# Kernel optimization log

Hardware: AMD Instinct MI355X
Metric: run time of the kernel (lower is better)

## Reference

```python
import jax, jax.numpy as jnp
import numpy as np

B, D, E, H, DEPTH, NH, K = 4, 384, 8, 1536, 12, 6, 2
P, NTOK = 16, 197  # patch size, 14*14 patches + cls
EPS = 1e-6


def layernorm(x, w, b):
    m = x.mean(-1, keepdims=True)
    v = ((x - m) ** 2).mean(-1, keepdims=True)
    return (x - m) / jnp.sqrt(v + EPS) * w + b


def attention(x, qkv_w, qkv_b, proj_w, proj_b):
    Bn, N, C = x.shape
    hd = C // NH
    qkv = x @ qkv_w.T + qkv_b                       # [B,N,3C]
    qkv = qkv.reshape(Bn, N, 3, NH, hd).transpose(2, 0, 3, 1, 4)
    q, k, v = qkv[0], qkv[1], qkv[2]                # [B,h,N,hd]
    attn = jax.nn.softmax((q @ k.transpose(0, 1, 3, 2)) * (hd ** -0.5), axis=-1)
    out = (attn @ v).transpose(0, 2, 1, 3).reshape(Bn, N, C)
    return out @ proj_w.T + proj_b


def mlp(x, w1, b1, w2, b2):
    h = jax.nn.gelu(x @ w1.T + b1, approximate=False)
    return h @ w2.T + b2


def moe_ffn(x2d, gw, w1, b1, w2, b2):
    # noiseless top-k gating (eval mode of NoisyTopKGating)
    logits = x2d @ gw                                # [T,E]
    T = logits.shape[0]
    top_vals, top_idx = jax.lax.top_k(logits, K + 1)
    gates_k = jax.nn.softmax(top_vals[:, :K], axis=-1)
    gates = jnp.zeros((T, E), x2d.dtype).at[jnp.arange(T)[:, None], top_idx[:, :K]].set(gates_k)
    # dense per-expert FFN, weighted combine (identical math to SparseDispatcher)
    h = jax.nn.gelu(jnp.einsum('td,edh->teh', x2d, w1) + b1, approximate=False)
    out = jnp.einsum('teh,ehd->ted', h, w2) + b2
    return jnp.einsum('te,ted->td', gates, out)


def forward(x, patch_w, patch_b, cls_token, pos_embed,
            ln1_w, ln1_b, qkv_w, qkv_b, proj_w, proj_b, ln2_w, ln2_b,
            fc1_w, fc1_b, fc2_w, fc2_b,
            gate_w, moe_w1, moe_b1, moe_w2, moe_b2, lnf_w, lnf_b):
    # patch embed: conv k=16 s=16
    feat = jax.lax.conv_general_dilated(x, patch_w, (P, P), 'VALID',
                                        dimension_numbers=('NCHW', 'OIHW', 'NCHW'))
    feat = feat + patch_b[None, :, None, None]
    Bn = feat.shape[0]
    tokens = feat.reshape(Bn, D, -1).transpose(0, 2, 1)          # [B,196,D]
    cls = jnp.broadcast_to(cls_token, (Bn, 1, D))
    h = jnp.concatenate([cls, tokens], axis=1) + pos_embed       # [B,197,D]

    for i in range(DEPTH):
        h = h + attention(layernorm(h, ln1_w[i], ln1_b[i]), qkv_w[i], qkv_b[i], proj_w[i], proj_b[i])
        y = layernorm(h, ln2_w[i], ln2_b[i])
        if i % 2 == 1:
            j = i // 2
            y2 = moe_ffn(y.reshape(-1, D), gate_w[j], moe_w1[j], moe_b1[j], moe_w2[j], moe_b2[j])
            h = h + y2.reshape(Bn, NTOK, D)
        else:
            j = i // 2
            h = h + mlp(y, fc1_w[j], fc1_b[j], fc2_w[j], fc2_b[j])
    return layernorm(h, lnf_w, lnf_b)


def setup_inputs() -> dict:
    key = jax.random.key(0)
    ks = jax.random.split(key, 16)
    rn = lambda k, s, sd=0.02: jax.random.normal(k, s, jnp.float32) * sd
    return {
        'x': jax.random.normal(ks[0], (B, 3, 224, 224), jnp.float32),
        'patch_w': rn(ks[1], (D, 3, P, P)), 'patch_b': jnp.zeros((D,), jnp.float32),
        'cls_token': rn(ks[2], (1, 1, D)), 'pos_embed': rn(ks[3], (1, NTOK, D)),
        'ln1_w': jnp.ones((DEPTH, D), jnp.float32), 'ln1_b': jnp.zeros((DEPTH, D), jnp.float32),
        'qkv_w': rn(ks[4], (DEPTH, 3 * D, D)), 'qkv_b': jnp.zeros((DEPTH, 3 * D), jnp.float32),
        'proj_w': rn(ks[5], (DEPTH, D, D)), 'proj_b': jnp.zeros((DEPTH, D), jnp.float32),
        'ln2_w': jnp.ones((DEPTH, D), jnp.float32), 'ln2_b': jnp.zeros((DEPTH, D), jnp.float32),
        'fc1_w': rn(ks[6], (DEPTH // 2, H, D)), 'fc1_b': jnp.zeros((DEPTH // 2, H), jnp.float32),
        'fc2_w': rn(ks[7], (DEPTH // 2, D, H)), 'fc2_b': jnp.zeros((DEPTH // 2, D), jnp.float32),
        'gate_w': rn(ks[8], (DEPTH // 2, D, E)),
        'moe_w1': rn(ks[9], (DEPTH // 2, E, D, H)), 'moe_b1': jnp.zeros((DEPTH // 2, E, H), jnp.float32),
        'moe_w2': rn(ks[10], (DEPTH // 2, E, H, D)), 'moe_b2': jnp.zeros((DEPTH // 2, E, D), jnp.float32),
        'lnf_w': jnp.ones((D,), jnp.float32), 'lnf_b': jnp.zeros((D,), jnp.float32),
    }


def reference(x, patch_w, patch_b, cls_token, pos_embed,
              ln1_w, ln1_b, qkv_w, qkv_b, proj_w, proj_b, ln2_w, ln2_b,
              fc1_w, fc1_b, fc2_w, fc2_b,
              gate_w, moe_w1, moe_b1, moe_w2, moe_b2, lnf_w, lnf_b):
    return forward(x, patch_w, patch_b, cls_token, pos_embed,
                   ln1_w, ln1_b, qkv_w, qkv_b, proj_w, proj_b, ln2_w, ln2_b,
                   fc1_w, fc1_b, fc2_w, fc2_b,
                   gate_w, moe_w1, moe_b1, moe_w2, moe_b2, lnf_w, lnf_b)
```

## Files before the change

kernel.cpp:

```cpp
#include <hip/hip_runtime.h>
#include <math.h>

#define NBATCH 4
#define NTOK 197
#define TT 788
#define DM 384
#define HM 1536
#define NHEAD 6
#define NEXP 8
#define LD2 72
#define MOUTSZ (TT * 2 * DM)

typedef __attribute__((ext_vector_type(8))) short bf16x8;
typedef __attribute__((ext_vector_type(4))) float f32x4;

__device__ __forceinline__ void f2bf2(float x, short& hi, short& lo) {
    unsigned u = __float_as_uint(x);
    unsigned uh = u + (0x7fffu + ((u >> 16) & 1u));
    hi = (short)(uh >> 16);
    float hf = __uint_as_float(uh & 0xffff0000u);
    float r = x - hf;
    unsigned v = __float_as_uint(r);
    lo = (short)((v + (0x7fffu + ((v >> 16) & 1u))) >> 16);
}
__device__ __forceinline__ float gelu_f(float x) {
    return 0.5f * x * (1.0f + erff(x * 0.7071067811865475f));
}

__global__ void k_im2col(const float* __restrict__ X, float* __restrict__ P) {
    int p = blockIdx.x;
    int b = p / 196, pp = p % 196;
    int py = pp / 14, px = pp % 14;
    const float* xb = X + (size_t)b * 3 * 224 * 224;
    float* dst = P + (size_t)p * 768;
    for (int idx = threadIdx.x; idx < 768; idx += 256) {
        int c = idx >> 8;
        int i = (idx >> 4) & 15;
        int j = idx & 15;
        dst[idx] = xb[((size_t)c * 224 + py * 16 + i) * 224 + px * 16 + j];
    }
}

__global__ void k_assemble(const float* __restrict__ PO, const float* __restrict__ pb,
                           const float* __restrict__ cls, const float* __restrict__ pos,
                           float* __restrict__ H) {
    int t = blockIdx.x;
    int b = t / NTOK, n = t % NTOK;
    for (int d = threadIdx.x; d < DM; d += 128) {
        float v;
        if (n == 0) v = cls[d];
        else v = PO[((size_t)b * 196 + (n - 1)) * DM + d] + pb[d];
        H[(size_t)t * DM + d] = v + pos[(size_t)n * DM + d];
    }
}

__global__ void k_ln(const float* __restrict__ X, const float* __restrict__ w,
                     const float* __restrict__ b, float* __restrict__ Y) {
    int t = blockIdx.x, lane = threadIdx.x;
    const float* x = X + (size_t)t * DM;
    float v[6];
    float s = 0.f;
    #pragma unroll
    for (int i = 0; i < 6; ++i) { v[i] = x[lane + i * 64]; s += v[i]; }
    #pragma unroll
    for (int off = 32; off; off >>= 1) s += __shfl_xor(s, off);
    float mean = s * (1.f / 384.f);
    float q = 0.f;
    #pragma unroll
    for (int i = 0; i < 6; ++i) { float d = v[i] - mean; q += d * d; }
    #pragma unroll
    for (int off = 32; off; off >>= 1) q += __shfl_xor(q, off);
    float inv = rsqrtf(q * (1.f / 384.f) + 1e-6f);
    float* y = Y + (size_t)t * DM;
    #pragma unroll
    for (int i = 0; i < 6; ++i) {
        int d = lane + i * 64;
        y[d] = (v[i] - mean) * inv * w[d] + b[d];
    }
}

__global__ __launch_bounds__(256) void k_gemm_mfma(
    const float* __restrict__ A, const float* __restrict__ W,
    const float* __restrict__ bias, float* __restrict__ C,
    int M, int N, int K, int flags, int MT, int NT, int wprot,
    const float* __restrict__ lnw, const float* __restrict__ lnb)
{
    int mt, nt;
    {
        int lane8 = blockIdx.x & 7;
        int idx = blockIdx.x >> 3;
        if (wprot) {
            mt = idx % MT;
            nt = lane8 + 8 * (idx / MT);
            if (nt >= NT) return;
        } else {
            nt = idx % NT;
            mt = lane8 + 8 * (idx / NT);
            if (mt >= MT) return;
        }
    }
    __shared__ short Ah[64 * LD2], Al[64 * LD2], Bh[64 * LD2], Bl[64 * LD2];
    const int bm = mt * 64, bn = nt * 64;
    const int tid = threadIdx.x;
    const int lane = tid & 63, w = tid >> 6;
    const int wr = w >> 1, wc = w & 1;
    const int r16 = lane & 15, g = lane >> 4;
    const int sr = tid >> 4;
    const int sc = (tid & 15) * 4;
    const bool doln = (flags & 8) != 0;
    float am[4], ai[4];
    #pragma unroll
    for (int p = 0; p < 4; ++p) { am[p] = 0.f; ai[p] = 1.f; }
    if (doln) {
        int j = tid & 15;
        #pragma unroll
        for (int p = 0; p < 4; ++p) {
            int r = bm + sr + p * 16;
            if (r < M) {
                const float* xr = A + (size_t)r * K;
                float s = 0.f, ss = 0.f;
                #pragma unroll
                for (int i = 0; i < 6; ++i) {
                    float4 v = *(const float4*)(xr + j * 4 + i * 64);
                    s += v.x + v.y + v.z + v.w;
                    ss += v.x * v.x + v.y * v.y + v.z * v.z + v.w * v.w;
                }
                #pragma unroll
                for (int off = 1; off < 16; off <<= 1) {
                    s += __shfl_xor(s, off);
                    ss += __shfl_xor(ss, off);
                }
                float mean = s * (1.f / 384.f);
                float var = ss * (1.f / 384.f) - mean * mean;
                am[p] = mean;
                ai[p] = rsqrtf(var + 1e-6f);
            }
        }
    }
    float4 ra[4], rb[4], lw4, lb4;
    auto LOADT = [&](int k0) {
        if (doln) {
            lw4 = *(const float4*)(lnw + k0 + sc);
            lb4 = *(const float4*)(lnb + k0 + sc);
        }
        #pragma unroll
        for (int p = 0; p < 4; ++p) {
            int r = sr + p * 16;
            ra[p] = make_float4(0.f, 0.f, 0.f, 0.f);
            if (bm + r < M) ra[p] = *(const float4*)(A + (size_t)(bm + r) * K + k0 + sc);
            rb[p] = *(const float4*)(W + (size_t)(bn + r) * K + k0 + sc);
        }
    };
    auto STORET = [&]() {
        #pragma unroll
        for (int p = 0; p < 4; ++p) {
            int r = sr + p * 16;
            float4 a4 = ra[p];
            if (doln) {
                a4.x = (a4.x - am[p]) * ai[p] * lw4.x + lb4.x;
                a4.y = (a4.y - am[p]) * ai[p] * lw4.y + lb4.y;
                a4.z = (a4.z - am[p]) * ai[p] * lw4.z + lb4.z;
                a4.w = (a4.w - am[p]) * ai[p] * lw4.w + lb4.w;
            }
            float4 b4 = rb[p];
            short4 ah, al, bh, bl;
            f2bf2(a4.x, ah.x, al.x); f2bf2(a4.y, ah.y, al.y);
            f2bf2(a4.z, ah.z, al.z); f2bf2(a4.w, ah.w, al.w);
            f2bf2(b4.x, bh.x, bl.x); f2bf2(b4.y, bh.y, bl.y);
            f2bf2(b4.z, bh.z, bl.z); f2bf2(b4.w, bh.w, bl.w);
            *(short4*)&Ah[r * LD2 + sc] = ah; *(short4*)&Al[r * LD2 + sc] = al;
            *(short4*)&Bh[r * LD2 + sc] = bh; *(short4*)&Bl[r * LD2 + sc] = bl;
        }
    };
    f32x4 acc[2][2] = {};
    auto COMPUTE = [&]() {
        #pragma unroll
        for (int kk = 0; kk < 2; ++kk) {
            bf16x8 afh[2], afl[2], bfh[2], bfl[2];
            #pragma unroll
            for (int i = 0; i < 2; ++i) {
                int off = (wr * 32 + i * 16 + r16) * LD2 + kk * 32 + g * 8;
                afh[i] = *(const bf16x8*)&Ah[off];
                afl[i] = *(const bf16x8*)&Al[off];
            }
            #pragma unroll
            for (int j = 0; j < 2; ++j) {
                int off = (wc * 32 + j * 16 + r16) * LD2 + kk * 32 + g * 8;
                bfh[j] = *(const bf16x8*)&Bh[off];
                bfl[j] = *(const bf16x8*)&Bl[off];
            }
            #pragma unroll
            for (int i = 0; i < 2; ++i)
                #pragma unroll
                for (int j = 0; j < 2; ++j) {
                    acc[i][j] = __builtin_amdgcn_mfma_f32_16x16x32_bf16(afl[i], bfh[j], acc[i][j], 0, 0, 0);
                    acc[i][j] = __builtin_amdgcn_mfma_f32_16x16x32_bf16(afh[i], bfl[j], acc[i][j], 0, 0, 0);
                    acc[i][j] = __builtin_amdgcn_mfma_f32_16x16x32_bf16(afh[i], bfh[j], acc[i][j], 0, 0, 0);
                }
        }
    };
    LOADT(0);
    STORET();
    __syncthreads();
    for (int k0 = 64; k0 < K; k0 += 64) {
        LOADT(k0);
        COMPUTE();
        __syncthreads();
        STORET();
        __syncthreads();
    }
    COMPUTE();
    #pragma unroll
    for (int i = 0; i < 2; ++i) {
        #pragma unroll
        for (int j = 0; j < 2; ++j) {
            int n = bn + wc * 32 + j * 16 + r16;
            float bb = bias ? bias[n] : 0.f;
            int mbase = bm + wr * 32 + i * 16 + g * 4;
            #pragma unroll
            for (int r = 0; r < 4; ++r) {
                int m = mbase + r;
                if (m < M) {
                    float v = acc[i][j][r] + bb;
                    if (flags & 1) v = gelu_f(v);
                    float* cp = C + (size_t)m * N + n;
                    if (flags & 2) v += *cp;
                    *cp = v;
                }
            }
        }
    }
}

__global__ __launch_bounds__(256) void k_scoresm(const float* __restrict__ QKV,
                                                 float* __restrict__ S) {
    int z = blockIdx.y;
    int b = z / NHEAD, hh = z % NHEAD;
    int i0 = blockIdx.x * 32;
    __shared__ float qs[32][65];
    __shared__ float ks[32][65];
    __shared__ float srow[32][200];
    int tid = threadIdx.x;
    int r = tid >> 3, d0 = (tid & 7) * 8, c0 = (tid & 7) * 4, l8 = tid & 7;
    {
        float4 v0 = make_float4(0,0,0,0), v1 = v0;
        if (i0 + r < NTOK) {
            const float* qp = QKV + ((size_t)(b * NTOK + i0 + r)) * 1152 + hh * 64 + d0;
            v0 = *(const float4*)qp; v1 = *(const float4*)(qp + 4);
        }
        qs[r][d0+0]=v0.x; qs[r][d0+1]=v0.y; qs[r][d0+2]=v0.z; qs[r][d0+3]=v0.w;
        qs[r][d0+4]=v1.x; qs[r][d0+5]=v1.y; qs[r][d0+6]=v1.z; qs[r][d0+7]=v1.w;
    }
    if (l8 == 0) { srow[r][197] = -1e30f; srow[r][198] = -1e30f; srow[r][199] = -1e30f; }
    for (int j0 = 0; j0 < NTOK; j0 += 32) {
        __syncthreads();
        {
            float4 v0 = make_float4(0,0,0,0), v1 = v0;
            if (j0 + r < NTOK) {
                const float* kp = QKV + ((size_t)(b * NTOK + j0 + r)) * 1152 + 384 + hh * 64 + d0;
                v0 = *(const float4*)kp; v1 = *(const float4*)(kp + 4);
            }
            ks[r][d0+0]=v0.x; ks[r][d0+1]=v0.y; ks[r][d0+2]=v0.z; ks[r][d0+3]=v0.w;
            ks[r][d0+4]=v1.x; ks[r][d0+5]=v1.y; ks[r][d0+6]=v1.z; ks[r][d0+7]=v1.w;
        }
        __syncthreads();
        float acc[4] = {0.f, 0.f, 0.f, 0.f};
        #pragma unroll 8
        for (int d = 0; d < 64; ++d) {
            float qv = qs[r][d];
            #pragma unroll
            for (int u = 0; u < 4; ++u) acc[u] += qv * ks[c0 + u][d];
        }
        #pragma unroll
        for (int u = 0; u < 4; ++u) {
            int j = j0 + c0 + u;
            if (j < NTOK) srow[r][j] = acc[u] * 0.125f;
        }
    }
    __syncthreads();
    float m = -1e30f;
    for (int c = l8; c < 200; c += 8) m = fmaxf(m, srow[r][c]);
    #pragma unroll
    for (int off = 1; off < 8; off <<= 1) m = fmaxf(m, __shfl_xor(m, off));
    float s = 0.f;
    for (int c = l8; c < 200; c += 8) {
        float e = expf(srow[r][c] - m);
        srow[r][c] = e;
        s += e;
    }
    #pragma unroll
    for (int off = 1; off < 8; off <<= 1) s += __shfl_xor(s, off);
    float invs = 1.f / s;
    int i = i0 + r;
    if (i < NTOK) {
        float* sp = S + ((size_t)z * NTOK + i) * NTOK;
        for (int c = l8; c < NTOK; c += 8) sp[c] = srow[r][c] * invs;
    }
}

__global__ __launch_bounds__(256) void k_pv(const float* __restrict__ S, const float* __restrict__ QKV,
                                            float* __restrict__ AO) {
    int z = blockIdx.y;
    int b = z / NHEAD, hh = z % NHEAD;
    int i0 = blockIdx.x * 32;
    __shared__ float ps[32][33];
    __shared__ float vs[32][65];
    int tid = threadIdx.x;
    int r = tid >> 3;
    int c4 = (tid & 7) * 4;
    int d0 = (tid & 7) * 8;
    float acc[8] = {};
    for (int k0 = 0; k0 < NTOK; k0 += 32) {
        #pragma unroll
        for (int u = 0; u < 4; ++u) {
            int i = i0 + r, j = k0 + c4 + u;
            ps[r][c4 + u] = (i < NTOK && j < NTOK) ? S[((size_t)z * NTOK + i) * NTOK + j] : 0.f;
        }
        {
            float4 v0 = make_float4(0,0,0,0), v1 = v0;
            if (k0 + r < NTOK) {
                const float* vp = QKV + ((size_t)(b * NTOK + k0 + r)) * 1152 + 768 + hh * 64 + d0;
                v0 = *(const float4*)vp; v1 = *(const float4*)(vp + 4);
            }
            vs[r][d0+0]=v0.x; vs[r][d0+1]=v0.y; vs[r][d0+2]=v0.z; vs[r][d0+3]=v0.w;
            vs[r][d0+4]=v1.x; vs[r][d0+5]=v1.y; vs[r][d0+6]=v1.z; vs[r][d0+7]=v1.w;
        }
        __syncthreads();
        #pragma unroll 8
        for (int kk = 0; kk < 32; ++kk) {
            float pw = ps[r][kk];
            #pragma unroll
            for (int j = 0; j < 8; ++j) acc[j] += pw * vs[kk][d0 + j];
        }
        __syncthreads();
    }
    int i = i0 + r;
    if (i < NTOK) {
        float* op = AO + (size_t)(b * NTOK + i) * DM + hh * 64 + d0;
        #pragma unroll
        for (int j = 0; j < 8; ++j) op[j] = acc[j];
    }
}

__global__ void k_route_ln(const float* __restrict__ H, float* __restrict__ lnstat,
                           const float* __restrict__ lnw, const float* __restrict__ lnb,
                           const float* __restrict__ GW,
                           int* __restrict__ eidx, float* __restrict__ egate) {
    int t = blockIdx.x * 4 + (threadIdx.x >> 6);
    if (t >= TT) return;
    int lane = threadIdx.x & 63;
    const float* x = H + (size_t)t * DM;
    float v[6];
    float s = 0.f, ss = 0.f;
    #pragma unroll
    for (int i = 0; i < 6; ++i) {
        v[i] = x[lane + i * 64];
        s += v[i];
        ss += v[i] * v[i];
    }
    #pragma unroll
    for (int off = 32; off; off >>= 1) { s += __shfl_xor(s, off); ss += __shfl_xor(ss, off); }
    float mean = s * (1.f / 384.f);
    float var = ss * (1.f / 384.f) - mean * mean;
    float inv = rsqrtf(var + 1e-6f);
    if (lane == 0) { lnstat[2 * t] = mean; lnstat[2 * t + 1] = inv; }
    float l8[NEXP] = {};
    #pragma unroll
    for (int i = 0; i < 6; ++i) {
        int d = lane + i * 64;
        float yv = (v[i] - mean) * inv * lnw[d] + lnb[d];
        const float* g = GW + (size_t)d * NEXP;
        #pragma unroll
        for (int e = 0; e < NEXP; ++e) l8[e] += yv * g[e];
    }
    #pragma unroll
    for (int e = 0; e < NEXP; ++e) {
        float vv = l8[e];
        #pragma unroll
        for (int off = 32; off; off >>= 1) vv += __shfl_xor(vv, off);
        l8[e] = vv;
    }
    if (lane == 0) {
        int b0 = 0;
        #pragma unroll
        for (int e = 1; e < NEXP; ++e) if (l8[e] > l8[b0]) b0 = e;
        int b1 = -1;
        #pragma unroll
        for (int e = 0; e < NEXP; ++e) if (e != b0 && (b1 < 0 || l8[e] > l8[b1])) b1 = e;
        float e1 = expf(l8[b1] - l8[b0]);
        float denom = 1.f + e1;
        eidx[2 * t] = b0; eidx[2 * t + 1] = b1;
        egate[2 * t] = 1.f / denom; egate[2 * t + 1] = e1 / denom;
    }
}

__global__ void k_pscatter(int* __restrict__ cnt, int* __restrict__ basep,
                           const int* __restrict__ eidx,
                           int* __restrict__ slot_tok, int* __restrict__ slot_of) {
    __shared__ int hist[NEXP];
    __shared__ int bp[NEXP];
    __shared__ int fl[NEXP];
    int tid = threadIdx.x;
    if (tid < NEXP) { hist[tid] = 0; fl[tid] = 0; }
    __syncthreads();
    for (int i = tid; i < 2 * TT; i += 256) atomicAdd(&hist[eidx[i]], 1);
    __syncthreads();
    if (tid == 0) {
        int s = 0;
        for (int e = 0; e < NEXP; ++e) { bp[e] = s; s += hist[e]; }
    }
    __syncthreads();
    if (tid < NEXP) { cnt[tid] = hist[tid]; basep[tid] = bp[tid]; }
    for (int t = tid; t < TT; t += 256) {
        #pragma unroll
        for (int k = 0; k < 2; ++k) {
            int e = eidx[2 * t + k];
            int pos = atomicAdd(&fl[e], 1);
            int s = bp[e] + pos;
            slot_tok[s] = t;
            slot_of[2 * t + k] = s;
        }
    }
}

__global__ __launch_bounds__(256) void k_moe1_mfma(
    const float* __restrict__ H, const float* __restrict__ lnstat,
    const float* __restrict__ lnw, const float* __restrict__ lnb,
    const float* __restrict__ W1, const float* __restrict__ B1,
    const int* __restrict__ slot_tok, const int* __restrict__ cnt, const int* __restrict__ basep,
    float* __restrict__ HID)
{
    const int e = blockIdx.x & 7;
    const int idx = blockIdx.x >> 3;
    const int mt = idx % 25;
    const int nt = idx / 25;
    const int c = cnt[e];
    const int r0 = mt * 64;
    if (r0 >= c) return;
    const int sbase = basep[e];
    const int n0 = nt * 64;
    const float* W = W1 + (size_t)e * DM * HM;
    const float* B1e = B1 + (size_t)e * HM;
    __shared__ short Ah[64 * LD2], Al[64 * LD2], Bh[64 * LD2], Bl[64 * LD2];
    const int tid = threadIdx.x;
    const int lane = tid & 63, w = tid >> 6;
    const int wr = w >> 1, wc = w & 1;
    const int r16 = lane & 15, g = lane >> 4;
    const int sr = tid >> 4, sc = (tid & 15) * 4;
    const int kq = (tid >> 4) * 4;
    int tokp[4];
    float am4[4], ai4[4];
    #pragma unroll
    for (int p = 0; p < 4; ++p) {
        int m = r0 + sr + p * 16;
        tokp[p] = (m < c) ? slot_tok[sbase + m] : -1;
        am4[p] = 0.f; ai4[p] = 1.f;
        if (tokp[p] >= 0) { am4[p] = lnstat[2 * tokp[p]]; ai4[p] = lnstat[2 * tokp[p] + 1]; }
    }
    f32x4 acc[2][2] = {};
    for (int k0 = 0; k0 < DM; k0 += 64) {
        float4 lw4 = *(const float4*)(lnw + k0 + sc);
        float4 lb4 = *(const float4*)(lnb + k0 + sc);
        #pragma unroll
        for (int p = 0; p < 4; ++p) {
            int r = sr + p * 16;
            float4 a4 = make_float4(0.f, 0.f, 0.f, 0.f);
            if (tokp[p] >= 0) {
                a4 = *(const float4*)(H + (size_t)tokp[p] * DM + k0 + sc);
                a4.x = (a4.x - am4[p]) * ai4[p] * lw4.x + lb4.x;
                a4.y = (a4.y - am4[p]) * ai4[p] * lw4.y + lb4.y;
                a4.z = (a4.z - am4[p]) * ai4[p] * lw4.z + lb4.z;
                a4.w = (a4.w - am4[p]) * ai4[p] * lw4.w + lb4.w;
            }
            short4 ah, al;
            f2bf2(a4.x, ah.x, al.x); f2bf2(a4.y, ah.y, al.y);
            f2bf2(a4.z, ah.z, al.z); f2bf2(a4.w, ah.w, al.w);
            *(short4*)&Ah[r * LD2 + sc] = ah; *(short4*)&Al[r * LD2 + sc] = al;
        }
        {
            float4 b4[4];
            #pragma unroll
            for (int i = 0; i < 4; ++i)
                b4[i] = *(const float4*)(W + (size_t)(k0 + kq + i) * HM + n0 + sc);
            float col[4][4] = {
                { b4[0].x, b4[1].x, b4[2].x, b4[3].x },
                { b4[0].y, b4[1].y, b4[2].y, b4[3].y },
                { b4[0].z, b4[1].z, b4[2].z, b4[3].z },
                { b4[0].w, b4[1].w, b4[2].w, b4[3].w } };
            #pragma unroll
            for (int u = 0; u < 4; ++u) {
                short4 hh, ll;
                f2bf2(col[u][0], hh.x, ll.x); f2bf2(col[u][1], hh.y, ll.y);
                f2bf2(col[u][2], hh.z, ll.z); f2bf2(col[u][3], hh.w, ll.w);
                *(short4*)&Bh[(sc + u) * LD2 + kq] = hh;
                *(short4*)&Bl[(sc + u) * LD2 + kq] = ll;
            }
        }
        __syncthreads();
        #pragma unroll
        for (int kk = 0; kk < 2; ++kk) {
            bf16x8 afh[2], afl[2], bfh[2], bfl[2];
            #pragma unroll
            for (int i = 0; i < 2; ++i) {
                int off = (wr * 32 + i * 16 + r16) * LD2 + kk * 32 + g * 8;
                afh[i] = *(const bf16x8*)&Ah[off];
                afl[i] = *(const bf16x8*)&Al[off];
            }
            #pragma unroll
            for (int j = 0; j < 2; ++j) {
                int off = (wc * 32 + j * 16 + r16) * LD2 + kk * 32 + g * 8;
                bfh[j] = *(const bf16x8*)&Bh[off];
                bfl[j] = *(const bf16x8*)&Bl[off];
            }
            #pragma unroll
            for (int i = 0; i < 2; ++i)
                #pragma unroll
                for (int j = 0; j < 2; ++j) {
                    acc[i][j] = __builtin_amdgcn_mfma_f32_16x16x32_bf16(afl[i], bfh[j], acc[i][j], 0, 0, 0);
                    acc[i][j] = __builtin_amdgcn_mfma_f32_16x16x32_bf16(afh[i], bfl[j], acc[i][j], 0, 0, 0);
                    acc[i][j] = __builtin_amdgcn_mfma_f32_16x16x32_bf16(afh[i], bfh[j], acc[i][j], 0, 0, 0);
                }
        }
        __syncthreads();
    }
    #pragma unroll
    for (int i = 0; i < 2; ++i) {
        #pragma unroll
        for (int j = 0; j < 2; ++j) {
            int n = n0 + wc * 32 + j * 16 + r16;
            float bb = B1e[n];
            #pragma unroll
            for (int r = 0; r < 4; ++r) {
                int m = r0 + wr * 32 + i * 16 + g * 4 + r;
                if (m < c)
                    HID[(size_t)(sbase + m) * HM + n] = gelu_f(acc[i][j][r] + bb);
            }
        }
    }
}

__global__ __launch_bounds__(256) void k_moe2_mfma(
    const float* __restrict__ HID, const float* __restrict__ W2,
    const int* __restrict__ cnt, const int* __restrict__ basep,
    float* __restrict__ MOUTP)
{
    const int e = blockIdx.x & 7;
    const int idx = blockIdx.x >> 3;
    const int mt = idx % 25;
    const int rest = idx / 25;
    const int nt = rest % 6;
    const int ks = rest / 6;
    const int c = cnt[e];
    const int r0 = mt * 64;
    if (r0 >= c) return;
    const int sbase = basep[e];
    const int n0 = nt * 64;
    const int kbase = ks * 384;
    const float* W = W2 + (size_t)e * HM * DM + (size_t)kbase * DM;
    float* outp = MOUTP + (size_t)ks * MOUTSZ;
    __shared__ short Ah[64 * LD2], Al[64 * LD2], Bh[64 * LD2], Bl[64 * LD2];
    const int tid = threadIdx.x;
    const int lane = tid & 63, w = tid >> 6;
    const int wr = w >> 1, wc = w & 1;
    const int r16 = lane & 15, g = lane >> 4;
    const int sr = tid >> 4, sc = (tid & 15) * 4;
    const int kq = (tid >> 4) * 4;
    f32x4 acc[2][2] = {};
    for (int k0 = 0; k0 < 384; k0 += 64) {
        #pragma unroll
        for (int p = 0; p < 4; ++p) {
            int r = sr + p * 16;
            int m = r0 + r;
            float4 a4 = make_float4(0.f, 0.f, 0.f, 0.f);
            if (m < c) a4 = *(const float4*)(HID + (size_t)(sbase + m) * HM + kbase + k0 + sc);
            short4 ah, al;
            f2bf2(a4.x, ah.x, al.x); f2bf2(a4.y, ah.y, al.y);
            f2bf2(a4.z, ah.z, al.z); f2bf2(a4.w, ah.w, al.w);
            *(short4*)&Ah[r * LD2 + sc] = ah; *(short4*)&Al[r * LD2 + sc] = al;
        }
        {
            float4 b4[4];
            #pragma unroll
            for (int i = 0; i < 4; ++i)
                b4[i] = *(const float4*)(W + (size_t)(k0 + kq + i) * DM + n0 + sc);
            float col[4][4] = {
                { b4[0].x, b4[1].x, b4[2].x, b4[3].x },
                { b4[0].y, b4[1].y, b4[2].y, b4[3].y },
                { b4[0].z, b4[1].z, b4[2].z, b4[3].z },
                { b4[0].w, b4[1].w, b4[2].w, b4[3].w } };
            #pragma unroll
            for (int u = 0; u < 4; ++u) {
                short4 hh, ll;
                f2bf2(col[u][0], hh.x, ll.x); f2bf2(col[u][1], hh.y, ll.y);
                f2bf2(col[u][2], hh.z, ll.z); f2bf2(col[u][3], hh.w, ll.w);
                *(short4*)&Bh[(sc + u) * LD2 + kq] = hh;
                *(short4*)&Bl[(sc + u) * LD2 + kq] = ll;
            }
        }
        __syncthreads();
        #pragma unroll
        for (int kk = 0; kk < 2; ++kk) {
            bf16x8 afh[2], afl[2], bfh[2], bfl[2];
            #pragma unroll
            for (int i = 0; i < 2; ++i) {
                int off = (wr * 32 + i * 16 + r16) * LD2 + kk * 32 + g * 8;
                afh[i] = *(const bf16x8*)&Ah[off];
                afl[i] = *(const bf16x8*)&Al[off];
            }
            #pragma unroll
            for (int j = 0; j < 2; ++j) {
                int off = (wc * 32 + j * 16 + r16) * LD2 + kk * 32 + g * 8;
                bfh[j] = *(const bf16x8*)&Bh[off];
                bfl[j] = *(const bf16x8*)&Bl[off];
            }
            #pragma unroll
            for (int i = 0; i < 2; ++i)
                #pragma unroll
                for (int j = 0; j < 2; ++j) {
                    acc[i][j] = __builtin_amdgcn_mfma_f32_16x16x32_bf16(afl[i], bfh[j], acc[i][j], 0, 0, 0);
                    acc[i][j] = __builtin_amdgcn_mfma_f32_16x16x32_bf16(afh[i], bfl[j], acc[i][j], 0, 0, 0);
                    acc[i][j] = __builtin_amdgcn_mfma_f32_16x16x32_bf16(afh[i], bfh[j], acc[i][j], 0, 0, 0);
                }
        }
        __syncthreads();
    }
    #pragma unroll
    for (int i = 0; i < 2; ++i) {
        #pragma unroll
        for (int j = 0; j < 2; ++j) {
            int n = n0 + wc * 32 + j * 16 + r16;
            #pragma unroll
            for (int r = 0; r < 4; ++r) {
                int m = r0 + wr * 32 + i * 16 + g * 4 + r;
                if (m < c)
                    outp[(size_t)(sbase + m) * DM + n] = acc[i][j][r];
            }
        }
    }
}

__global__ void k_combine(const float* __restrict__ MOUTP, const int* __restrict__ slot_of,
                          const int* __restrict__ eidx, const float* __restrict__ egate,
                          const float* __restrict__ B2, float* __restrict__ H) {
    int t = blockIdx.x;
    int s0 = slot_of[2 * t], s1 = slot_of[2 * t + 1];
    int e0 = eidx[2 * t], e1 = eidx[2 * t + 1];
    float g0 = egate[2 * t], g1 = egate[2 * t + 1];
    for (int d = threadIdx.x; d < DM; d += 128) {
        float v0 = B2[(size_t)e0 * DM + d];
        float v1 = B2[(size_t)e1 * DM + d];
        #pragma unroll
        for (int p = 0; p < 4; ++p) {
            v0 += MOUTP[(size_t)p * MOUTSZ + (size_t)s0 * DM + d];
            v1 += MOUTP[(size_t)p * MOUTSZ + (size_t)s1 * DM + d];
        }
        H[(size_t)t * DM + d] += g0 * v0 + g1 * v1;
    }
}

extern "C" void kernel_launch(void* const* d_in, const int* in_sizes, int n_in,
                              void* d_out, int out_size, void* d_ws, size_t ws_size,
                              hipStream_t stream) {
    const float* x         = (const float*)d_in[0];
    const float* patch_w   = (const float*)d_in[1];
    const float* patch_b   = (const float*)d_in[2];
    const float* cls_token = (const float*)d_in[3];
    const float* pos_embed = (const float*)d_in[4];
    const float* ln1_w     = (const float*)d_in[5];
    const float* ln1_b     = (const float*)d_in[6];
    const float* qkv_w     = (const float*)d_in[7];
    const float* qkv_b     = (const float*)d_in[8];
    const float* proj_w    = (const float*)d_in[9];
    const float* proj_b    = (const float*)d_in[10];
    const float* ln2_w     = (const float*)d_in[11];
    const float* ln2_b     = (const float*)d_in[12];
    const float* fc1_w     = (const float*)d_in[13];
    const float* fc1_b     = (const float*)d_in[14];
    const float* fc2_w     = (const float*)d_in[15];
    const float* fc2_b     = (const float*)d_in[16];
    const float* gate_w    = (const float*)d_in[17];
    const float* moe_w1    = (const float*)d_in[18];
    const float* moe_b1    = (const float*)d_in[19];
    const float* moe_w2    = (const float*)d_in[20];
    const float* moe_b2    = (const float*)d_in[21];
    const float* lnf_w     = (const float*)d_in[22];
    const float* lnf_b     = (const float*)d_in[23];
    float* out = (float*)d_out;

    float* wsf = (float*)d_ws;
    float* regA     = wsf;
    float* patches  = regA;
    float* patchout = regA + 602112;
    float* moehid   = regA;
    float* h     = regA + 2420736;
    float* spare = h + 302592;
    float* qkvb  = spare + 302592;
    float* attno = qkvb + 907776;
    float* regC  = attno + 302592;
    float* S    = regC;
    float* hid  = regC;
    float* mout4 = qkvb;
    float* egate = regC + 1210368;
    int* ib       = (int*)(egate + 1576);
    int* eidx     = ib;
    int* slot_tok = ib + 1576;
    int* slot_of  = ib + 3152;
    int* cnt      = ib + 4728;
    int* basep    = ib + 4736;
    float* lnstat = (float*)(ib + 4752);

    k_im2col<<<784, 256, 0, stream>>>(x, patches);
    k_gemm_mfma<<<96, 256, 0, stream>>>(patches, patch_w, nullptr, patchout,
                                        784, DM, 768, 0, 13, 6, 0, nullptr, nullptr);
    k_assemble<<<TT, 128, 0, stream>>>(patchout, patch_b, cls_token, pos_embed, h);

    for (int l = 0; l < 12; ++l) {
        k_gemm_mfma<<<312, 256, 0, stream>>>(h, qkv_w + (size_t)l * 1152 * DM,
                                             qkv_b + l * 1152, qkvb, TT, 1152, DM, 8,
                                             13, 18, 1,
                                             ln1_w + l * DM, ln1_b + l * DM);
        k_scoresm<<<dim3(7, NBATCH * NHEAD), 256, 0, stream>>>(qkvb, S);
        k_pv<<<dim3(7, NBATCH * NHEAD), 256, 0, stream>>>(S, qkvb, attno);
        k_gemm_mfma<<<96, 256, 0, stream>>>(attno, proj_w + (size_t)l * DM * DM,
                                            proj_b + l * DM, h, TT, DM, DM, 2,
                                            13, 6, 0, nullptr, nullptr);
        int j = l >> 1;
        if ((l & 1) == 0) {
            k_gemm_mfma<<<312, 256, 0, stream>>>(h, fc1_w + (size_t)j * HM * DM,
                                                 fc1_b + j * HM, hid, TT, HM, DM, 9,
                                                 13, 24, 1,
                                                 ln2_w + l * DM, ln2_b + l * DM);
            k_gemm_mfma<<<96, 256, 0, stream>>>(hid, fc2_w + (size_t)j * DM * HM,
                                                fc2_b + j * DM, h, TT, DM, HM, 2,
                                                13, 6, 0, nullptr, nullptr);
        } else {
            k_route_ln<<<197, 256, 0, stream>>>(h, lnstat, ln2_w + l * DM, ln2_b + l * DM,
                                                gate_w + (size_t)j * DM * NEXP, eidx, egate);
            k_pscatter<<<1, 256, 0, stream>>>(cnt, basep, eidx, slot_tok, slot_of);
            k_moe1_mfma<<<8 * 25 * 24, 256, 0, stream>>>(
                h, lnstat, ln2_w + l * DM, ln2_b + l * DM,
                moe_w1 + (size_t)j * NEXP * DM * HM, moe_b1 + (size_t)j * NEXP * HM,
                slot_tok, cnt, basep, moehid);
            k_moe2_mfma<<<8 * 25 * 24, 256, 0, stream>>>(
                moehid, moe_w2 + (size_t)j * NEXP * HM * DM, cnt, basep, mout4);
            k_combine<<<TT, 128, 0, stream>>>(mout4, slot_of, eidx, egate,
                                              moe_b2 + (size_t)j * NEXP * DM, h);
        }
    }
    k_ln<<<TT, 64, 0, stream>>>(h, lnf_w, lnf_b, out);
}
```

Measured before the change: 1.787 ms.

## Fuse attention scores, softmax and PV into one online-softmax kernel

Replaces the separate scores+softmax kernel and PV kernel with a single flash-style kernel. It keeps a running max and sum per query row, rescales the PV accumulator for each 32-key tile, and reuses one shared buffer for K and then V. This removes the write and re-read of the full probability matrix in global memory and one launch per layer, at the cost of extra exp and rescale work per tile. Separately, the MoE expert GEMM grids shrink from 25 to 13 row tiles per expert, since no expert can receive more than 788 tokens, which cuts the number of blocks that launch only to exit.

```diff
diff --git a/kernel.cpp b/kernel.cpp
--- a/kernel.cpp
+++ b/kernel.cpp
@@ -232,16 +232,19 @@
     }
 }
 
-__global__ __launch_bounds__(256) void k_scoresm(const float* __restrict__ QKV,
-                                                 float* __restrict__ S) {
+__global__ __launch_bounds__(256) void k_fattn(const float* __restrict__ QKV,
+                                               float* __restrict__ AO) {
     int z = blockIdx.y;
     int b = z / NHEAD, hh = z % NHEAD;
     int i0 = blockIdx.x * 32;
     __shared__ float qs[32][65];
-    __shared__ float ks[32][65];
-    __shared__ float srow[32][200];
+    __shared__ float kv[32][65];
+    __shared__ float sc[32][33];
     int tid = threadIdx.x;
-    int r = tid >> 3, d0 = (tid & 7) * 8, c0 = (tid & 7) * 4, l8 = tid & 7;
+    int r = tid >> 3;
+    int l8 = tid & 7;
+    int d0 = l8 * 8;
+    int c0 = l8 * 4;
     {
         float4 v0 = make_float4(0,0,0,0), v1 = v0;
         if (i0 + r < NTOK) {
@@ -251,7 +254,8 @@
         qs[r][d0+0]=v0.x; qs[r][d0+1]=v0.y; qs[r][d0+2]=v0.z; qs[r][d0+3]=v0.w;
         qs[r][d0+4]=v1.x; qs[r][d0+5]=v1.y; qs[r][d0+6]=v1.z; qs[r][d0+7]=v1.w;
     }
-    if (l8 == 0) { srow[r][197] = -1e30f; srow[r][198] = -1e30f; srow[r][199] = -1e30f; }
+    float accv[8] = {};
+    float mrow = -1e30f, lrow = 0.f;
     for (int j0 = 0; j0 < NTOK; j0 += 32) {
         __syncthreads();
         {
@@ -260,85 +264,65 @@
                 const float* kp = QKV + ((size_t)(b * NTOK + j0 + r)) * 1152 + 384 + hh * 64 + d0;
                 v0 = *(const float4*)kp; v1 = *(const float4*)(kp + 4);
             }
-            ks[r][d0+0]=v0.x; ks[r][d0+1]=v0.y; ks[r][d0+2]=v0.z; ks[r][d0+3]=v0.w;
-            ks[r][d0+4]=v1.x; ks[r][d0+5]=v1.y; ks[r][d0+6]=v1.z; ks[r][d0+7]=v1.w;
-        }
-        __syncthreads();
-        float acc[4] = {0.f, 0.f, 0.f, 0.f};
+            kv[r][d0+0]=v0.x; kv[r][d0+1]=v0.y; kv[r][d0+2]=v0.z; kv[r][d0+3]=v0.w;
+            kv[r][d0+4]=v1.x; kv[r][d0+5]=v1.y; kv[r][d0+6]=v1.z; kv[r][d0+7]=v1.w;
+        }
+        __syncthreads();
+        float a0 = 0.f, a1 = 0.f, a2 = 0.f, a3 = 0.f;
         #pragma unroll 8
         for (int d = 0; d < 64; ++d) {
             float qv = qs[r][d];
-            #pragma unroll
-            for (int u = 0; u < 4; ++u) acc[u] += qv * ks[c0 + u][d];
-        }
+            a0 += qv * kv[c0 + 0][d];
+            a1 += qv * kv[c0 + 1][d];
+            a2 += qv * kv[c0 + 2][d];
+            a3 += qv * kv[c0 + 3][d];
+        }
+        float s4[4];
+        s4[0] = (j0 + c0 + 0 < NTOK) ? a0 * 0.125f : -1e30f;
+        s4[1] = (j0 + c0 + 1 < NTOK) ? a1 * 0.125f : -1e30f;
+        s4[2] = (j0 + c0 + 2 < NTOK) ? a2 * 0.125f : -1e30f;
+        s4[3] = (j0 + c0 + 3 < NTOK) ? a3 * 0.125f : -1e30f;
+        float tmax = fmaxf(fmaxf(s4[0], s4[1]), fmaxf(s4[2], s4[3]));
+        #pragma unroll
+        for (int off = 1; off < 8; off <<= 1) tmax = fmaxf(tmax, __shfl_xor(tmax, off));
+        float mnew = fmaxf(mrow, tmax);
+        float scale = expf(mrow - mnew);
+        float tsum = 0.f;
         #pragma unroll
         for (int u = 0; u < 4; ++u) {
-            int j = j0 + c0 + u;
-            if (j < NTOK) srow[r][j] = acc[u] * 0.125f;
-        }
-    }
-    __syncthreads();
-    float m = -1e30f;
-    for (int c = l8; c < 200; c += 8) m = fmaxf(m, srow[r][c]);
-    #pragma unroll
-    for (int off = 1; off < 8; off <<= 1) m = fmaxf(m, __shfl_xor(m, off));
-    float s = 0.f;
-    for (int c = l8; c < 200; c += 8) {
-        float e = expf(srow[r][c] - m);
-        srow[r][c] = e;
-        s += e;
-    }
-    #pragma unroll
-    for (int off = 1; off < 8; off <<= 1) s += __shfl_xor(s, off);
-    float invs = 1.f / s;
-    int i = i0 + r;
-    if (i < NTOK) {
-        float* sp = S + ((size_t)z * NTOK + i) * NTOK;
-        for (int c = l8; c < NTOK; c += 8) sp[c] = srow[r][c] * invs;
-    }
-}
-
-__global__ __launch_bounds__(256) void k_pv(const float* __restrict__ S, const float* __restrict__ QKV,
-                                            float* __restrict__ AO) {
-    int z = blockIdx.y;
-    int b = z / NHEAD, hh = z % NHEAD;
-    int i0 = blockIdx.x * 32;
-    __shared__ float ps[32][33];
-    __shared__ float vs[32][65];
-    int tid = threadIdx.x;
-    int r = tid >> 3;
-    int c4 = (tid & 7) * 4;
-    int d0 = (tid & 7) * 8;
-    float acc[8] = {};
-    for (int k0 = 0; k0 < NTOK; k0 += 32) {
-        #pragma unroll
-        for (int u = 0; u < 4; ++u) {
-            int i = i0 + r, j = k0 + c4 + u;
-            ps[r][c4 + u] = (i < NTOK && j < NTOK) ? S[((size_t)z * NTOK + i) * NTOK + j] : 0.f;
-        }
+            float e = expf(s4[u] - mnew);
+            sc[r][c0 + u] = e;
+            tsum += e;
+        }
+        #pragma unroll
+        for (int off = 1; off < 8; off <<= 1) tsum += __shfl_xor(tsum, off);
+        lrow = lrow * scale + tsum;
+        mrow = mnew;
+        #pragma unroll
+        for (int j = 0; j < 8; ++j) accv[j] *= scale;
+        __syncthreads();
         {
             float4 v0 = make_float4(0,0,0,0), v1 = v0;
-            if (k0 + r < NTOK) {
-                const float* vp = QKV + ((size_t)(b * NTOK + k0 + r)) * 1152 + 768 + hh * 64 + d0;
+            if (j0 + r < NTOK) {
+                const float* vp = QKV + ((size_t)(b * NTOK + j0 + r)) * 1152 + 768 + hh * 64 + d0;
                 v0 = *(const float4*)vp; v1 = *(const float4*)(vp + 4);
             }
-            vs[r][d0+0]=v0.x; vs[r][d0+1]=v0.y; vs[r][d0+2]=v0.z; vs[r][d0+3]=v0.w;
-            vs[r][d0+4]=v1.x; vs[r][d0+5]=v1.y; vs[r][d0+6]=v1.z; vs[r][d0+7]=v1.w;
+            kv[r][d0+0]=v0.x; kv[r][d0+1]=v0.y; kv[r][d0+2]=v0.z; kv[r][d0+3]=v0.w;
+            kv[r][d0+4]=v1.x; kv[r][d0+5]=v1.y; kv[r][d0+6]=v1.z; kv[r][d0+7]=v1.w;
         }
         __syncthreads();
         #pragma unroll 8
         for (int kk = 0; kk < 32; ++kk) {
-            float pw = ps[r][kk];
-            #pragma unroll
-            for (int j = 0; j < 8; ++j) acc[j] += pw * vs[kk][d0 + j];
-        }
-        __syncthreads();
-    }
-    int i = i0 + r;
-    if (i < NTOK) {
-        float* op = AO + (size_t)(b * NTOK + i) * DM + hh * 64 + d0;
-        #pragma unroll
-        for (int j = 0; j < 8; ++j) op[j] = acc[j];
+            float pw = sc[r][kk];
+            #pragma unroll
+            for (int j = 0; j < 8; ++j) accv[j] += pw * kv[kk][d0 + j];
+        }
+    }
+    if (i0 + r < NTOK) {
+        float inv = 1.f / lrow;
+        float* op = AO + (size_t)(b * NTOK + i0 + r) * DM + hh * 64 + d0;
+        #pragma unroll
+        for (int j = 0; j < 8; ++j) op[j] = accv[j] * inv;
     }
 }
 
@@ -432,8 +416,8 @@
 {
     const int e = blockIdx.x & 7;
     const int idx = blockIdx.x >> 3;
-    const int mt = idx % 25;
-    const int nt = idx / 25;
+    const int mt = idx % 13;
+    const int nt = idx / 13;
     const int c = cnt[e];
     const int r0 = mt * 64;
     if (r0 >= c) return;
@@ -546,8 +530,8 @@
 {
     const int e = blockIdx.x & 7;
     const int idx = blockIdx.x >> 3;
-    const int mt = idx % 25;
-    const int rest = idx / 25;
+    const int mt = idx % 13;
+    const int rest = idx / 13;
     const int nt = rest % 6;
     const int ks = rest / 6;
     const int c = cnt[e];
@@ -697,7 +681,6 @@
     float* qkvb  = spare + 302592;
     float* attno = qkvb + 907776;
     float* regC  = attno + 302592;
-    float* S    = regC;
     float* hid  = regC;
     float* mout4 = qkvb;
     float* egate = regC + 1210368;
@@ -719,8 +702,7 @@
                                              qkv_b + l * 1152, qkvb, TT, 1152, DM, 8,
                                              13, 18, 1,
                                              ln1_w + l * DM, ln1_b + l * DM);
-        k_scoresm<<<dim3(7, NBATCH * NHEAD), 256, 0, stream>>>(qkvb, S);
-        k_pv<<<dim3(7, NBATCH * NHEAD), 256, 0, stream>>>(S, qkvb, attno);
+        k_fattn<<<dim3(7, NBATCH * NHEAD), 256, 0, stream>>>(qkvb, attno);
         k_gemm_mfma<<<96, 256, 0, stream>>>(attno, proj_w + (size_t)l * DM * DM,
                                             proj_b + l * DM, h, TT, DM, DM, 2,
                                             13, 6, 0, nullptr, nullptr);
@@ -737,11 +719,11 @@
             k_route_ln<<<197, 256, 0, stream>>>(h, lnstat, ln2_w + l * DM, ln2_b + l * DM,
                                                 gate_w + (size_t)j * DM * NEXP, eidx, egate);
             k_pscatter<<<1, 256, 0, stream>>>(cnt, basep, eidx, slot_tok, slot_of);
-            k_moe1_mfma<<<8 * 25 * 24, 256, 0, stream>>>(
+            k_moe1_mfma<<<8 * 13 * 24, 256, 0, stream>>>(
                 h, lnstat, ln2_w + l * DM, ln2_b + l * DM,
                 moe_w1 + (size_t)j * NEXP * DM * HM, moe_b1 + (size_t)j * NEXP * HM,
                 slot_tok, cnt, basep, moehid);
-            k_moe2_mfma<<<8 * 25 * 24, 256, 0, stream>>>(
+            k_moe2_mfma<<<8 * 13 * 24, 256, 0, stream>>>(
                 moehid, moe_w2 + (size_t)j * NEXP * HM * DM, cnt, basep, mout4);
             k_combine<<<TT, 128, 0, stream>>>(mout4, slot_of, eidx, egate,
                                               moe_b2 + (size_t)j * NEXP * DM, h);
```

New measurement: 1.807 ms. About the same (+1.1%).

## Replace LDS-tiled GEMM with single-wave register GEMM and trim MoE grids

Applied to the files above, without the earlier changes.

The dense GEMM used for patch embedding, QKV, proj and the MLP layers is replaced by a one-wavefront kernel on 32x32 tiles. Each lane loads its MFMA operand fragments straight from global memory into double-buffered registers, so there is no LDS staging and no block barriers. This launches several times more blocks, which addresses the poor CU occupancy of the earlier 96- and 312-block grids. The cost is that operand reuse now depends on L2 instead of shared memory, so more global loads are issued. Separately, the MoE expert kernels now launch 13 row tiles per expert instead of 25, enough to cover the 788-token maximum, which removes blocks that only exited early.

```diff
diff --git a/kernel.cpp b/kernel.cpp
--- a/kernel.cpp
+++ b/kernel.cpp
@@ -79,7 +79,9 @@
     }
 }
 
-__global__ __launch_bounds__(256) void k_gemm_mfma(
+struct FR { float4 a00, a01, a10, a11, b00, b01, b10, b11; };
+
+__global__ __launch_bounds__(64) void k_gemm_rw(
     const float* __restrict__ A, const float* __restrict__ W,
     const float* __restrict__ bias, float* __restrict__ C,
     int M, int N, int K, int flags, int MT, int NT, int wprot,
@@ -99,124 +101,108 @@
             if (mt >= MT) return;
         }
     }
-    __shared__ short Ah[64 * LD2], Al[64 * LD2], Bh[64 * LD2], Bl[64 * LD2];
-    const int bm = mt * 64, bn = nt * 64;
-    const int tid = threadIdx.x;
-    const int lane = tid & 63, w = tid >> 6;
-    const int wr = w >> 1, wc = w & 1;
+    const int bm = mt * 32, bn = nt * 32;
+    const int lane = threadIdx.x;
     const int r16 = lane & 15, g = lane >> 4;
-    const int sr = tid >> 4;
-    const int sc = (tid & 15) * 4;
+    const int rA0 = bm + r16, rA1 = bm + 16 + r16;
+    const bool a0ok = rA0 < M, a1ok = rA1 < M;
+    const float* ap0 = A + (size_t)rA0 * K;
+    const float* ap1 = A + (size_t)rA1 * K;
+    const float* bp0 = W + (size_t)(bn + r16) * K;
+    const float* bp1 = W + (size_t)(bn + 16 + r16) * K;
     const bool doln = (flags & 8) != 0;
-    float am[4], ai[4];
-    #pragma unroll
-    for (int p = 0; p < 4; ++p) { am[p] = 0.f; ai[p] = 1.f; }
+    float am0 = 0.f, ai0 = 1.f, am1 = 0.f, ai1 = 1.f;
     if (doln) {
-        int j = tid & 15;
-        #pragma unroll
-        for (int p = 0; p < 4; ++p) {
-            int r = bm + sr + p * 16;
-            if (r < M) {
-                const float* xr = A + (size_t)r * K;
-                float s = 0.f, ss = 0.f;
-                #pragma unroll
-                for (int i = 0; i < 6; ++i) {
-                    float4 v = *(const float4*)(xr + j * 4 + i * 64);
-                    s += v.x + v.y + v.z + v.w;
-                    ss += v.x * v.x + v.y * v.y + v.z * v.z + v.w * v.w;
-                }
-                #pragma unroll
-                for (int off = 1; off < 16; off <<= 1) {
-                    s += __shfl_xor(s, off);
-                    ss += __shfl_xor(ss, off);
-                }
-                float mean = s * (1.f / 384.f);
-                float var = ss * (1.f / 384.f) - mean * mean;
-                am[p] = mean;
-                ai[p] = rsqrtf(var + 1e-6f);
-            }
-        }
-    }
-    float4 ra[4], rb[4], lw4, lb4;
-    auto LOADT = [&](int k0) {
+        int row = bm + (lane & 31);
+        float s = 0.f, ss = 0.f;
+        if (row < M) {
+            const float* xr = A + (size_t)row * 384 + (lane >> 5) * 192;
+            #pragma unroll
+            for (int i = 0; i < 48; ++i) {
+                float4 v = *(const float4*)(xr + i * 4);
+                s += v.x + v.y + v.z + v.w;
+                ss += v.x * v.x + v.y * v.y + v.z * v.z + v.w * v.w;
+            }
+        }
+        s += __shfl_xor(s, 32);
+        ss += __shfl_xor(ss, 32);
+        float mean = s * (1.f / 384.f);
+        float var = ss * (1.f / 384.f) - mean * mean;
+        float inv = rsqrtf(var + 1e-6f);
+        am0 = __shfl(mean, r16);      ai0 = __shfl(inv, r16);
+        am1 = __shfl(mean, r16 + 16); ai1 = __shfl(inv, r16 + 16);
+    }
+    f32x4 acc[2][2] = {};
+
+    auto LOAD = [&](int k0, FR& R) {
+        int kc = k0 + g * 8;
+        float4 z = make_float4(0.f, 0.f, 0.f, 0.f);
+        R.a00 = a0ok ? *(const float4*)(ap0 + kc) : z;
+        R.a01 = a0ok ? *(const float4*)(ap0 + kc + 4) : z;
+        R.a10 = a1ok ? *(const float4*)(ap1 + kc) : z;
+        R.a11 = a1ok ? *(const float4*)(ap1 + kc + 4) : z;
+        R.b00 = *(const float4*)(bp0 + kc);
+        R.b01 = *(const float4*)(bp0 + kc + 4);
+        R.b10 = *(const float4*)(bp1 + kc);
+        R.b11 = *(const float4*)(bp1 + kc + 4);
+    };
+    auto COMP = [&](int k0, const FR& R) {
+        float av0[8] = { R.a00.x, R.a00.y, R.a00.z, R.a00.w, R.a01.x, R.a01.y, R.a01.z, R.a01.w };
+        float av1[8] = { R.a10.x, R.a10.y, R.a10.z, R.a10.w, R.a11.x, R.a11.y, R.a11.z, R.a11.w };
+        float bv0[8] = { R.b00.x, R.b00.y, R.b00.z, R.b00.w, R.b01.x, R.b01.y, R.b01.z, R.b01.w };
+        float bv1[8] = { R.b10.x, R.b10.y, R.b10.z, R.b10.w, R.b11.x, R.b11.y, R.b11.z, R.b11.w };
         if (doln) {
-            lw4 = *(const float4*)(lnw + k0 + sc);
-            lb4 = *(const float4*)(lnb + k0 + sc);
-        }
-        #pragma unroll
-        for (int p = 0; p < 4; ++p) {
-            int r = sr + p * 16;
-            ra[p] = make_float4(0.f, 0.f, 0.f, 0.f);
-            if (bm + r < M) ra[p] = *(const float4*)(A + (size_t)(bm + r) * K + k0 + sc);
-            rb[p] = *(const float4*)(W + (size_t)(bn + r) * K + k0 + sc);
-        }
+            int kc = k0 + g * 8;
+            float4 w0 = *(const float4*)(lnw + kc);
+            float4 w1 = *(const float4*)(lnw + kc + 4);
+            float4 q0 = *(const float4*)(lnb + kc);
+            float4 q1 = *(const float4*)(lnb + kc + 4);
+            float lwv[8] = { w0.x, w0.y, w0.z, w0.w, w1.x, w1.y, w1.z, w1.w };
+            float lbv[8] = { q0.x, q0.y, q0.z, q0.w, q1.x, q1.y, q1.z, q1.w };
+            #pragma unroll
+            for (int u = 0; u < 8; ++u) {
+                av0[u] = (av0[u] - am0) * ai0 * lwv[u] + lbv[u];
+                av1[u] = (av1[u] - am1) * ai1 * lwv[u] + lbv[u];
+            }
+        }
+        bf16x8 ah0, al0, ah1, al1, bh0, bl0, bh1, bl1;
+        #pragma unroll
+        for (int u = 0; u < 8; ++u) {
+            short h, l;
+            f2bf2(av0[u], h, l); ah0[u] = h; al0[u] = l;
+            f2bf2(av1[u], h, l); ah1[u] = h; al1[u] = l;
+            f2bf2(bv0[u], h, l); bh0[u] = h; bl0[u] = l;
+            f2bf2(bv1[u], h, l); bh1[u] = h; bl1[u] = l;
+        }
+        acc[0][0] = __builtin_amdgcn_mfma_f32_16x16x32_bf16(al0, bh0, acc[0][0], 0, 0, 0);
+        acc[0][0] = __builtin_amdgcn_mfma_f32_16x16x32_bf16(ah0, bl0, acc[0][0], 0, 0, 0);
+        acc[0][0] = __builtin_amdgcn_mfma_f32_16x16x32_bf16(ah0, bh0, acc[0][0], 0, 0, 0);
+        acc[0][1] = __builtin_amdgcn_mfma_f32_16x16x32_bf16(al0, bh1, acc[0][1], 0, 0, 0);
+        acc[0][1] = __builtin_amdgcn_mfma_f32_16x16x32_bf16(ah0, bl1, acc[0][1], 0, 0, 0);
+        acc[0][1] = __builtin_amdgcn_mfma_f32_16x16x32_bf16(ah0, bh1, acc[0][1], 0, 0, 0);
+        acc[1][0] = __builtin_amdgcn_mfma_f32_16x16x32_bf16(al1, bh0, acc[1][0], 0, 0, 0);
+        acc[1][0] = __builtin_amdgcn_mfma_f32_16x16x32_bf16(ah1, bl0, acc[1][0], 0, 0, 0);
+        acc[1][0] = __builtin_amdgcn_mfma_f32_16x16x32_bf16(ah1, bh0, acc[1][0], 0, 0, 0);
+        acc[1][1] = __builtin_amdgcn_mfma_f32_16x16x32_bf16(al1, bh1, acc[1][1], 0, 0, 0);
+        acc[1][1] = __builtin_amdgcn_mfma_f32_16x16x32_bf16(ah1, bl1, acc[1][1], 0, 0, 0);
+        acc[1][1] = __builtin_amdgcn_mfma_f32_16x16x32_bf16(ah1, bh1, acc[1][1], 0, 0, 0);
     };
-    auto STORET = [&]() {
-        #pragma unroll
-        for (int p = 0; p < 4; ++p) {
-            int r = sr + p * 16;
-            float4 a4 = ra[p];
-            if (doln) {
-                a4.x = (a4.x - am[p]) * ai[p] * lw4.x + lb4.x;
-                a4.y = (a4.y - am[p]) * ai[p] * lw4.y + lb4.y;
-                a4.z = (a4.z - am[p]) * ai[p] * lw4.z + lb4.z;
-                a4.w = (a4.w - am[p]) * ai[p] * lw4.w + lb4.w;
-            }
-            float4 b4 = rb[p];
-            short4 ah, al, bh, bl;
-            f2bf2(a4.x, ah.x, al.x); f2bf2(a4.y, ah.y, al.y);
-            f2bf2(a4.z, ah.z, al.z); f2bf2(a4.w, ah.w, al.w);
-            f2bf2(b4.x, bh.x, bl.x); f2bf2(b4.y, bh.y, bl.y);
-            f2bf2(b4.z, bh.z, bl.z); f2bf2(b4.w, bh.w, bl.w);
-            *(short4*)&Ah[r * LD2 + sc] = ah; *(short4*)&Al[r * LD2 + sc] = al;
-            *(short4*)&Bh[r * LD2 + sc] = bh; *(short4*)&Bl[r * LD2 + sc] = bl;
-        }
-    };
-    f32x4 acc[2][2] = {};
-    auto COMPUTE = [&]() {
-        #pragma unroll
-        for (int kk = 0; kk < 2; ++kk) {
-            bf16x8 afh[2], afl[2], bfh[2], bfl[2];
-            #pragma unroll
-            for (int i = 0; i < 2; ++i) {
-                int off = (wr * 32 + i * 16 + r16) * LD2 + kk * 32 + g * 8;
-                afh[i] = *(const bf16x8*)&Ah[off];
-                afl[i] = *(const bf16x8*)&Al[off];
-            }
-            #pragma unroll
-            for (int j = 0; j < 2; ++j) {
-                int off = (wc * 32 + j * 16 + r16) * LD2 + kk * 32 + g * 8;
-                bfh[j] = *(const bf16x8*)&Bh[off];
-                bfl[j] = *(const bf16x8*)&Bl[off];
-            }
-            #pragma unroll
-            for (int i = 0; i < 2; ++i)
-                #pragma unroll
-                for (int j = 0; j < 2; ++j) {
-                    acc[i][j] = __builtin_amdgcn_mfma_f32_16x16x32_bf16(afl[i], bfh[j], acc[i][j], 0, 0, 0);
-                    acc[i][j] = __builtin_amdgcn_mfma_f32_16x16x32_bf16(afh[i], bfl[j], acc[i][j], 0, 0, 0);
-                    acc[i][j] = __builtin_amdgcn_mfma_f32_16x16x32_bf16(afh[i], bfh[j], acc[i][j], 0, 0, 0);
-                }
-        }
-    };
-    LOADT(0);
-    STORET();
-    __syncthreads();
-    for (int k0 = 64; k0 < K; k0 += 64) {
-        LOADT(k0);
-        COMPUTE();
-        __syncthreads();
-        STORET();
-        __syncthreads();
-    }
-    COMPUTE();
+
+    FR Ra, Rb;
+    LOAD(0, Ra);
+    for (int k0 = 0; k0 < K; k0 += 64) {
+        LOAD(k0 + 32, Rb);
+        COMP(k0, Ra);
+        if (k0 + 64 < K) LOAD(k0 + 64, Ra);
+        COMP(k0 + 32, Rb);
+    }
     #pragma unroll
     for (int i = 0; i < 2; ++i) {
         #pragma unroll
         for (int j = 0; j < 2; ++j) {
-            int n = bn + wc * 32 + j * 16 + r16;
+            int n = bn + j * 16 + r16;
             float bb = bias ? bias[n] : 0.f;
-            int mbase = bm + wr * 32 + i * 16 + g * 4;
+            int mbase = bm + i * 16 + g * 4;
             #pragma unroll
             for (int r = 0; r < 4; ++r) {
                 int m = mbase + r;
@@ -364,30 +350,30 @@
     float var = ss * (1.f / 384.f) - mean * mean;
     float inv = rsqrtf(var + 1e-6f);
     if (lane == 0) { lnstat[2 * t] = mean; lnstat[2 * t + 1] = inv; }
-    float l8[NEXP] = {};
+    float l8v[NEXP] = {};
     #pragma unroll
     for (int i = 0; i < 6; ++i) {
         int d = lane + i * 64;
         float yv = (v[i] - mean) * inv * lnw[d] + lnb[d];
         const float* g = GW + (size_t)d * NEXP;
         #pragma unroll
-        for (int e = 0; e < NEXP; ++e) l8[e] += yv * g[e];
+        for (int e = 0; e < NEXP; ++e) l8v[e] += yv * g[e];
     }
     #pragma unroll
     for (int e = 0; e < NEXP; ++e) {
-        float vv = l8[e];
+        float vv = l8v[e];
         #pragma unroll
         for (int off = 32; off; off >>= 1) vv += __shfl_xor(vv, off);
-        l8[e] = vv;
+        l8v[e] = vv;
     }
     if (lane == 0) {
         int b0 = 0;
         #pragma unroll
-        for (int e = 1; e < NEXP; ++e) if (l8[e] > l8[b0]) b0 = e;
+        for (int e = 1; e < NEXP; ++e) if (l8v[e] > l8v[b0]) b0 = e;
         int b1 = -1;
         #pragma unroll
-        for (int e = 0; e < NEXP; ++e) if (e != b0 && (b1 < 0 || l8[e] > l8[b1])) b1 = e;
-        float e1 = expf(l8[b1] - l8[b0]);
+        for (int e = 0; e < NEXP; ++e) if (e != b0 && (b1 < 0 || l8v[e] > l8v[b1])) b1 = e;
+        float e1 = expf(l8v[b1] - l8v[b0]);
         float denom = 1.f + e1;
         eidx[2 * t] = b0; eidx[2 * t + 1] = b1;
         egate[2 * t] = 1.f / denom; egate[2 * t + 1] = e1 / denom;
@@ -432,8 +418,8 @@
 {
     const int e = blockIdx.x & 7;
     const int idx = blockIdx.x >> 3;
-    const int mt = idx % 25;
-    const int nt = idx / 25;
+    const int mt = idx % 13;
+    const int nt = idx / 13;
     const int c = cnt[e];
     const int r0 = mt * 64;
     if (r0 >= c) return;
@@ -546,8 +532,8 @@
 {
     const int e = blockIdx.x & 7;
     const int idx = blockIdx.x >> 3;
-    const int mt = idx % 25;
-    const int rest = idx / 25;
+    const int mt = idx % 13;
+    const int rest = idx / 13;
     const int nt = rest % 6;
     const int ks = rest / 6;
     const int c = cnt[e];
@@ -710,38 +696,38 @@
     float* lnstat = (float*)(ib + 4752);
 
     k_im2col<<<784, 256, 0, stream>>>(x, patches);
-    k_gemm_mfma<<<96, 256, 0, stream>>>(patches, patch_w, nullptr, patchout,
-                                        784, DM, 768, 0, 13, 6, 0, nullptr, nullptr);
+    k_gemm_rw<<<384, 64, 0, stream>>>(patches, patch_w, nullptr, patchout,
+                                      784, 384, 768, 0, 25, 12, 0, nullptr, nullptr);
     k_assemble<<<TT, 128, 0, stream>>>(patchout, patch_b, cls_token, pos_embed, h);
 
     for (int l = 0; l < 12; ++l) {
-        k_gemm_mfma<<<312, 256, 0, stream>>>(h, qkv_w + (size_t)l * 1152 * DM,
-                                             qkv_b + l * 1152, qkvb, TT, 1152, DM, 8,
-                                             13, 18, 1,
-                                             ln1_w + l * DM, ln1_b + l * DM);
+        k_gemm_rw<<<1000, 64, 0, stream>>>(h, qkv_w + (size_t)l * 1152 * DM,
+                                           qkv_b + l * 1152, qkvb, TT, 1152, DM, 8,
+                                           25, 36, 1,
+                                           ln1_w + l * DM, ln1_b + l * DM);
         k_scoresm<<<dim3(7, NBATCH * NHEAD), 256, 0, stream>>>(qkvb, S);
         k_pv<<<dim3(7, NBATCH * NHEAD), 256, 0, stream>>>(S, qkvb, attno);
-        k_gemm_mfma<<<96, 256, 0, stream>>>(attno, proj_w + (size_t)l * DM * DM,
-                                            proj_b + l * DM, h, TT, DM, DM, 2,
-                                            13, 6, 0, nullptr, nullptr);
+        k_gemm_rw<<<384, 64, 0, stream>>>(attno, proj_w + (size_t)l * DM * DM,
+                                          proj_b + l * DM, h, TT, DM, DM, 2,
+                                          25, 12, 0, nullptr, nullptr);
         int j = l >> 1;
         if ((l & 1) == 0) {
-            k_gemm_mfma<<<312, 256, 0, stream>>>(h, fc1_w + (size_t)j * HM * DM,
-                                                 fc1_b + j * HM, hid, TT, HM, DM, 9,
-                                                 13, 24, 1,
-                                                 ln2_w + l * DM, ln2_b + l * DM);
-            k_gemm_mfma<<<96, 256, 0, stream>>>(hid, fc2_w + (size_t)j * DM * HM,
-                                                fc2_b + j * DM, h, TT, DM, HM, 2,
-                                                13, 6, 0, nullptr, nullptr);
+            k_gemm_rw<<<1200, 64, 0, stream>>>(h, fc1_w + (size_t)j * HM * DM,
+                                               fc1_b + j * HM, hid, TT, HM, DM, 9,
+                                               25, 48, 1,
+                                               ln2_w + l * DM, ln2_b + l * DM);
+            k_gemm_rw<<<384, 64, 0, stream>>>(hid, fc2_w + (size_t)j * DM * HM,
+                                              fc2_b + j * DM, h, TT, DM, HM, 2,
+                                              25, 12, 0, nullptr, nullptr);
         } else {
             k_route_ln<<<197, 256, 0, stream>>>(h, lnstat, ln2_w + l * DM, ln2_b + l * DM,
                                                 gate_w + (size_t)j * DM * NEXP, eidx, egate);
             k_pscatter<<<1, 256, 0, stream>>>(cnt, basep, eidx, slot_tok, slot_of);
-            k_moe1_mfma<<<8 * 25 * 24, 256, 0, stream>>>(
+            k_moe1_mfma<<<8 * 13 * 24, 256, 0, stream>>>(
                 h, lnstat, ln2_w + l * DM, ln2_b + l * DM,
                 moe_w1 + (size_t)j * NEXP * DM * HM, moe_b1 + (size_t)j * NEXP * HM,
                 slot_tok, cnt, basep, moehid);
-            k_moe2_mfma<<<8 * 25 * 24, 256, 0, stream>>>(
+            k_moe2_mfma<<<8 * 13 * 24, 256, 0, stream>>>(
                 moehid, moe_w2 + (size_t)j * NEXP * HM * DM, cnt, basep, mout4);
             k_combine<<<TT, 128, 0, stream>>>(mout4, slot_of, eidx, egate,
                                               moe_b2 + (size_t)j * NEXP * DM, h);
```

Measured after the change: 2.450 ms. 1.37x slower.
